# Optimization experiments

Measured on AMD Instinct MI355X. Metric: run time of the kernel, lower is better.

The kernel has to match this reference:

```python
import jax, jax.numpy as jnp
import numpy as np

B_GRAPHS = 2048      # number of source graphs
N_CAND = 524288      # total candidate rows (~256 per graph)
EMB = 128            # emb_dim
HID = 256            # mlp_nb_hidden


def setup_inputs() -> dict:
    key = jax.random.key(0)
    ks = jax.random.split(key, 8)
    g_emb = jax.random.normal(ks[0], (B_GRAPHS, EMB), jnp.float32)
    cand_emb = jax.random.normal(ks[1], (N_CAND, EMB), jnp.float32)
    batch_idx = jnp.sort(jax.random.randint(ks[2], (N_CAND,), 0, B_GRAPHS, dtype=jnp.int32))
    def lin(k, fan_in, fan_out):
        return jax.random.normal(k, (fan_in, fan_out), jnp.float32) * (1.0 / np.sqrt(fan_in))
    W1 = lin(ks[3], 2 * EMB, HID); b1 = jnp.zeros((HID,), jnp.float32)
    W2 = lin(ks[4], HID, HID);     b2 = jnp.zeros((HID,), jnp.float32)
    W3 = lin(ks[5], HID, HID);     b3 = jnp.zeros((HID,), jnp.float32)
    Wf = lin(ks[6], HID, 1);       bf = jnp.zeros((1,), jnp.float32)
    return {"g_emb": g_emb, "cand_emb": cand_emb, "W1": W1, "b1": b1,
            "W2": W2, "b2": b2, "W3": W3, "b3": b3, "Wf": Wf, "bf": bf,
            "batch_idx": batch_idx}


def reference(g_emb, cand_emb, W1, b1, W2, b2, W3, b3, Wf, bf, batch_idx):
    B = g_emb.shape[0]
    # repeat_interleave(g_emb, bincount(batch_idx)) == gather by batch_idx (batch_idx sorted)
    X = jnp.concatenate([g_emb[batch_idx], cand_emb], axis=1)  # [N, 2*EMB]
    X_states = X
    h = jax.nn.relu(X @ W1 + b1)
    h = jax.nn.relu(h @ W2 + b2)
    h = jax.nn.relu(h @ W3 + b3)
    logits = (h @ Wf + bf)[:, 0]  # [N]
    # batched_softmax: exp -> segment (global_add_pool) sum -> gather -> divide
    e = jnp.exp(logits)
    denom = jax.ops.segment_sum(e, batch_idx, num_segments=B)  # [B]
    probs = e / denom[batch_idx]
    # eval-mode forward returns (g_emb, X_states, probs)
    return (g_emb, X_states, probs)
```

## Files before the change

kernel.cpp:

```cpp
#include <hip/hip_runtime.h>
#include <hip/hip_bf16.h>
#include <math.h>

#define N_CAND 524288
#define RB     128
#define NBLK   (N_CAND / RB)
#define EMB    128
#define HID    256
#define BGR    2048

#define OUT_XS  262144
#define OUT_P   (262144 + 134217728)

typedef __attribute__((ext_vector_type(4))) float f32x4;
typedef __attribute__((ext_vector_type(8))) short bf16x8;
typedef __attribute__((ext_vector_type(4))) short bf16x4;
typedef unsigned short u16;

__device__ __forceinline__ u16 f2bf(float f) {
  __hip_bfloat16 h = __float2bfloat16(f);
  return *reinterpret_cast<u16*>(&h);
}

__device__ __forceinline__ void bar_lgkm() {
  __builtin_amdgcn_sched_barrier(0);
  asm volatile("s_waitcnt lgkmcnt(0)" ::: "memory");
  __builtin_amdgcn_sched_barrier(0);
  __builtin_amdgcn_s_barrier();
  __builtin_amdgcn_sched_barrier(0);
}
__device__ __forceinline__ void bar_only() {
  __builtin_amdgcn_sched_barrier(0);
  __builtin_amdgcn_s_barrier();
  __builtin_amdgcn_sched_barrier(0);
}

__global__ void k_prep(const float* __restrict__ W1, const float* __restrict__ W2,
                       const float* __restrict__ W3, u16* __restrict__ wt) {
  const int b = blockIdx.x;
  const int m = b >> 8;
  const int n = b & 255;
  const int k = threadIdx.x;
  const float* W = (m == 0) ? W1 : ((m == 1) ? W2 : W3);
  const int nt = n >> 4, ml = n & 15;
  const int ks = k >> 5, g = (k >> 3) & 3, j = k & 7;
  const int lane = g * 16 + ml;
  wt[(((m * 16 + nt) * 8 + ks) << 9) + lane * 8 + j] = f2bf(W[k * 256 + n]);
}

__device__ __forceinline__ void mlp_layer(
    int Lidx, u16* buf, const u16* __restrict__ wt, const float* bias_s,
    int w, int lane, int ml, int g, int wn0, int swz, int bofs)
{
  const char* wl = (const char*)wt +
      ((size_t)(Lidx * 16 + w * 2) * 8) * 1024 + lane * 16;
  const float* bs = bias_s + Lidx * HID;
  char* const hb  = (char*)buf;
  char* const hbr = hb + (size_t)ml * 512;

  f32x4 acc[2][8];
  #pragma unroll
  for (int nf = 0; nf < 2; ++nf)
    #pragma unroll
    for (int rf = 0; rf < 8; ++rf)
      acc[nf][rf] = (f32x4){0.f, 0.f, 0.f, 0.f};

  __builtin_amdgcn_s_setprio(1);
  #pragma unroll
  for (int ks = 0; ks < 8; ++ks) {
    bf16x8 a[2];
    #pragma unroll
    for (int nf = 0; nf < 2; ++nf)
      a[nf] = *(const bf16x8*)(wl + (nf * 8 + ks) * 1024);
    #pragma unroll
    for (int rh = 0; rh < 2; ++rh) {
      bf16x8 bq[4];
      #pragma unroll
      for (int rj = 0; rj < 4; ++rj)
        bq[rj] = *(const bf16x8*)(hbr + (rh * 4 + rj) * 8192 + ((ks * 64) ^ bofs));
      #pragma unroll
      for (int nf = 0; nf < 2; ++nf)
        #pragma unroll
        for (int rj = 0; rj < 4; ++rj)
          acc[nf][rh * 4 + rj] = __builtin_amdgcn_mfma_f32_16x16x32_bf16(
              a[nf], bq[rj], acc[nf][rh * 4 + rj], 0, 0, 0);
    }
  }
  __builtin_amdgcn_s_setprio(0);
  bar_only();

  #pragma unroll
  for (int nf = 0; nf < 2; ++nf) {
    const int n0 = wn0 + nf * 16 + g * 4;
    const f32x4 bb = *(const f32x4*)(bs + n0);
    #pragma unroll
    for (int rf = 0; rf < 8; ++rf) {
      const int r = rf * 16 + ml;
      bf16x4 hv;
      #pragma unroll
      for (int q = 0; q < 4; ++q) {
        float x = acc[nf][rf][q] + bb[q];
        x = fmaxf(x, 0.f);
        hv[q] = (short)f2bf(x);
      }
      *(bf16x4*)(hb + r * 512 + ((n0 * 2) ^ swz)) = hv;
    }
  }
  bar_lgkm();
}

__global__ __launch_bounds__(512, 4) void k_main(
    const float* __restrict__ g_emb, const float* __restrict__ cand,
    const int* __restrict__ bidx,
    const float* __restrict__ b1, const float* __restrict__ b2,
    const float* __restrict__ b3, const float* __restrict__ Wf,
    const float* __restrict__ bfp, const u16* __restrict__ wt,
    float* __restrict__ out)
{
  __shared__ __align__(16) u16 hbuf[RB * HID];
  __shared__ float bias_s[3 * HID];
  __shared__ float bf_s;

  const int tid = threadIdx.x;
  const int r0  = blockIdx.x * RB;

  if (tid < HID) {
    bias_s[tid]           = b1[tid];
    bias_s[HID + tid]     = b2[tid];
    bias_s[2 * HID + tid] = b3[tid];
    if (tid == 0) bf_s = bfp[0];
  }

  {
    const int kc   = tid & 31;
    const int row0 = tid >> 5;
    char* l0 = (char*)hbuf;
    int bpre[8];
    #pragma unroll
    for (int i = 0; i < 8; ++i)
      bpre[i] = bidx[r0 + row0 + i * 16];
    #pragma unroll
    for (int i = 0; i < 8; ++i) {
      const int row = row0 + i * 16;
      const int r   = r0 + row;
      const float* src = (kc < 16)
          ? g_emb + (size_t)bpre[i] * EMB + kc * 8
          : cand  + (size_t)r * EMB + (kc - 16) * 8;
      f32x4 v0 = *(const f32x4*)(src);
      f32x4 v1 = *(const f32x4*)(src + 4);
      float* dst = out + OUT_XS + (size_t)r * (2 * EMB) + kc * 8;
      __builtin_nontemporal_store(v0, (f32x4*)dst);
      __builtin_nontemporal_store(v1, (f32x4*)(dst + 4));
      bf16x8 hv;
      hv[0] = (short)f2bf(v0.x); hv[1] = (short)f2bf(v0.y);
      hv[2] = (short)f2bf(v0.z); hv[3] = (short)f2bf(v0.w);
      hv[4] = (short)f2bf(v1.x); hv[5] = (short)f2bf(v1.y);
      hv[6] = (short)f2bf(v1.z); hv[7] = (short)f2bf(v1.w);
      *(bf16x8*)(l0 + row * 512 + ((kc * 16) ^ ((row & 15) << 4))) = hv;
    }
  }
  bar_lgkm();

  const int lane = tid & 63;
  const int w    = tid >> 6;
  const int ml   = lane & 15;
  const int g    = lane >> 4;
  const int wn0  = w * 32;

  const int swz  = ml << 4;
  const int bofs = (g * 16) ^ swz;
  char* const hb  = (char*)hbuf;
  const char* const hbr = hb + (size_t)ml * 512;

  mlp_layer(0, hbuf, wt, bias_s, w, lane, ml, g, wn0, swz, bofs);
  mlp_layer(1, hbuf, wt, bias_s, w, lane, ml, g, wn0, swz, bofs);

  {
    const char* wl = (const char*)wt +
        ((size_t)(2 * 16 + w * 2) * 8) * 1024 + lane * 16;

    f32x4 acc[2][8];
    #pragma unroll
    for (int nf = 0; nf < 2; ++nf)
      #pragma unroll
      for (int rf = 0; rf < 8; ++rf)
        acc[nf][rf] = (f32x4){0.f, 0.f, 0.f, 0.f};

    __builtin_amdgcn_s_setprio(1);
    #pragma unroll
    for (int ks = 0; ks < 8; ++ks) {
      bf16x8 a[2];
      #pragma unroll
      for (int nf = 0; nf < 2; ++nf)
        a[nf] = *(const bf16x8*)(wl + (nf * 8 + ks) * 1024);
      #pragma unroll
      for (int rh = 0; rh < 2; ++rh) {
        bf16x8 bq[4];
        #pragma unroll
        for (int rj = 0; rj < 4; ++rj)
          bq[rj] = *(const bf16x8*)(hbr + (rh * 4 + rj) * 8192 + ((ks * 64) ^ bofs));
        #pragma unroll
        for (int nf = 0; nf < 2; ++nf)
          #pragma unroll
          for (int rj = 0; rj < 4; ++rj)
            acc[nf][rh * 4 + rj] = __builtin_amdgcn_mfma_f32_16x16x32_bf16(
                a[nf], bq[rj], acc[nf][rh * 4 + rj], 0, 0, 0);
      }
    }
    __builtin_amdgcn_s_setprio(0);
    bar_only();

    const float* bs = bias_s + 2 * HID;
    const f32x4 bb0 = *(const f32x4*)(bs + wn0 + g * 4);
    const f32x4 bb1 = *(const f32x4*)(bs + wn0 + 16 + g * 4);
    const f32x4 wf0 = *(const f32x4*)(Wf + wn0 + g * 4);
    const f32x4 wf1 = *(const f32x4*)(Wf + wn0 + 16 + g * 4);

    float* pad = (float*)hbuf;
    #pragma unroll
    for (int rf = 0; rf < 8; ++rf) {
      const int r = rf * 16 + ml;
      f32x4 x0 = acc[0][rf] + bb0;
      f32x4 x1 = acc[1][rf] + bb1;
      float p = 0.f;
      #pragma unroll
      for (int q = 0; q < 4; ++q) {
        p += fmaxf(x0[q], 0.f) * wf0[q];
        p += fmaxf(x1[q], 0.f) * wf1[q];
      }
      const int slot = (w * 4 + g) ^ ((r & 7) << 2);
      pad[r * 32 + slot] = p;
    }
    bar_lgkm();

    {
      const int row  = tid >> 2;
      const int part = tid & 3;
      const int sx   = (row & 7) << 2;
      f32x4 v0 = *(const f32x4*)(pad + row * 32 + ((part * 8) ^ sx));
      f32x4 v1 = *(const f32x4*)(pad + row * 32 + ((part * 8 + 4) ^ sx));
      float s = v0[0] + v0[1] + v0[2] + v0[3] + v1[0] + v1[1] + v1[2] + v1[3];
      s += __shfl_xor(s, 1);
      s += __shfl_xor(s, 2);
      if (part == 0)
        out[OUT_P + (size_t)(r0 + row)] = __expf(s + bf_s);
    }
  }
}

__global__ __launch_bounds__(256) void k_soft(
    const float* __restrict__ g_emb, const int* __restrict__ bidx,
    float* __restrict__ out)
{
  const int b   = blockIdx.x;
  const int tid = threadIdx.x;
  __shared__ float ws[4];
  __shared__ float sden;

  int lo = 0, hi = N_CAND;
  while (lo < hi) { int m = (lo + hi) >> 1; if (bidx[m] < b) lo = m + 1; else hi = m; }
  int lo2 = lo, hi2 = N_CAND;
  while (lo2 < hi2) { int m = (lo2 + hi2) >> 1; if (bidx[m] < b + 1) lo2 = m + 1; else hi2 = m; }

  float s = 0.f;
  for (int i = lo + tid; i < lo2; i += 256) s += out[OUT_P + (size_t)i];
  #pragma unroll
  for (int off = 32; off > 0; off >>= 1) s += __shfl_down(s, off);
  if ((tid & 63) == 0) ws[tid >> 6] = s;
  __syncthreads();
  if (tid == 0) sden = ws[0] + ws[1] + ws[2] + ws[3];
  __syncthreads();
  const float d = sden;
  for (int i = lo + tid; i < lo2; i += 256)
    out[OUT_P + (size_t)i] = out[OUT_P + (size_t)i] / d;

  if (tid < 32) {
    f32x4 v = *(const f32x4*)(g_emb + (size_t)b * EMB + tid * 4);
    *(f32x4*)(out + (size_t)b * EMB + tid * 4) = v;
  }
}

extern "C" void kernel_launch(void* const* d_in, const int* in_sizes, int n_in,
                              void* d_out, int out_size, void* d_ws, size_t ws_size,
                              hipStream_t stream)
{
  const float* g_emb = (const float*)d_in[0];
  const float* cand  = (const float*)d_in[1];
  const float* W1    = (const float*)d_in[2];
  const float* b1    = (const float*)d_in[3];
  const float* W2    = (const float*)d_in[4];
  const float* b2    = (const float*)d_in[5];
  const float* W3    = (const float*)d_in[6];
  const float* b3    = (const float*)d_in[7];
  const float* Wf    = (const float*)d_in[8];
  const float* bfp   = (const float*)d_in[9];
  const int*   bidx  = (const int*)d_in[10];
  float* out = (float*)d_out;

  u16* wt = (u16*)d_ws;

  k_prep <<<768, 256, 0, stream>>>(W1, W2, W3, wt);
  k_main <<<NBLK, 512, 0, stream>>>(g_emb, cand, bidx, b1, b2, b3, Wf, bfp, wt, out);
  k_soft <<<BGR, 256, 0, stream>>>(g_emb, bidx, out);
}
```

Baseline: 275.8 us.

## Split X_states copy into dedicated blocks interleaved with MLP blocks

The grid is reorganized into groups of five blocks: four compute blocks each run the MLP on 128 rows, and a fifth block copies the 512-row X_states slice (gathered graph embedding plus candidate embedding) to the output. Compute blocks no longer issue the large nontemporal stores, which should shorten their critical path and let memory-bound copy blocks overlap with MFMA-bound compute blocks. In exchange the input rows are read twice (once by the copy block, once by the compute block), adding global read traffic.

```diff
diff --git a/kernel.cpp b/kernel.cpp
--- a/kernel.cpp
+++ b/kernel.cpp
@@ -5,6 +5,7 @@
 #define N_CAND 524288
 #define RB     128
 #define NBLK   (N_CAND / RB)
+#define NG     1024
 #define EMB    128
 #define HID    256
 #define BGR    2048
@@ -122,7 +123,41 @@
   __shared__ float bf_s;
 
   const int tid = threadIdx.x;
-  const int r0  = blockIdx.x * RB;
+  const int gid = blockIdx.x / 5;
+  const int sub = blockIdx.x % 5;
+
+  if (sub == 4) {
+    const int kc    = tid & 31;
+    const int row0  = tid >> 5;
+    const int rbase = gid * 512;
+    if (kc < 16) {
+      #pragma unroll 4
+      for (int i = 0; i < 32; ++i) {
+        const int r = rbase + row0 + i * 16;
+        const int b = bidx[r];
+        const float* src = g_emb + (size_t)b * EMB + kc * 8;
+        f32x4 v0 = *(const f32x4*)src;
+        f32x4 v1 = *(const f32x4*)(src + 4);
+        float* dst = out + OUT_XS + (size_t)r * (2 * EMB) + kc * 8;
+        __builtin_nontemporal_store(v0, (f32x4*)dst);
+        __builtin_nontemporal_store(v1, (f32x4*)(dst + 4));
+      }
+    } else {
+      #pragma unroll 4
+      for (int i = 0; i < 32; ++i) {
+        const int r = rbase + row0 + i * 16;
+        const float* src = cand + (size_t)r * EMB + (kc - 16) * 8;
+        f32x4 v0 = *(const f32x4*)src;
+        f32x4 v1 = *(const f32x4*)(src + 4);
+        float* dst = out + OUT_XS + (size_t)r * (2 * EMB) + kc * 8;
+        __builtin_nontemporal_store(v0, (f32x4*)dst);
+        __builtin_nontemporal_store(v1, (f32x4*)(dst + 4));
+      }
+    }
+    return;
+  }
+
+  const int r0 = (gid * 4 + sub) * RB;
 
   if (tid < HID) {
     bias_s[tid]           = b1[tid];
@@ -148,9 +183,6 @@
           : cand  + (size_t)r * EMB + (kc - 16) * 8;
       f32x4 v0 = *(const f32x4*)(src);
       f32x4 v1 = *(const f32x4*)(src + 4);
-      float* dst = out + OUT_XS + (size_t)r * (2 * EMB) + kc * 8;
-      __builtin_nontemporal_store(v0, (f32x4*)dst);
-      __builtin_nontemporal_store(v1, (f32x4*)(dst + 4));
       bf16x8 hv;
       hv[0] = (short)f2bf(v0.x); hv[1] = (short)f2bf(v0.y);
       hv[2] = (short)f2bf(v0.z); hv[3] = (short)f2bf(v0.w);
@@ -300,6 +332,6 @@
   u16* wt = (u16*)d_ws;
 
   k_prep <<<768, 256, 0, stream>>>(W1, W2, W3, wt);
-  k_main <<<NBLK, 512, 0, stream>>>(g_emb, cand, bidx, b1, b2, b3, Wf, bfp, wt, out);
+  k_main <<<5 * NG, 512, 0, stream>>>(g_emb, cand, bidx, b1, b2, b3, Wf, bfp, wt, out);
   k_soft <<<BGR, 256, 0, stream>>>(g_emb, bidx, out);
 }
```

Measured after the change: 295.8 us. 1.07x slower.
